# Kernel tuning notes

Hardware: AMD Instinct MI355X
Metric: run time of the kernel (lower is better)

The kernel has to match this reference:

```python
import math
import jax, jax.numpy as jnp
import numpy as np

B, S, E, H, DK, NW = 2048, 1, 1024, 128, 8, 8  # d_k == n_wires == 8, seq_len must be 1
DIM = 2 ** NW


def setup_inputs() -> dict:
    key = jax.random.key(0)
    ks = jax.random.split(key, 7)
    scale = 1.0 / math.sqrt(E)
    return {
        "x": jax.random.normal(ks[0], (B, S, E), jnp.float32),
        "wq": jax.random.normal(ks[1], (E, E), jnp.float32) * scale,
        "wk": jax.random.normal(ks[2], (E, E), jnp.float32) * scale,
        "wv": jax.random.normal(ks[3], (E, E), jnp.float32) * scale,
        "wc": jax.random.normal(ks[4], (E, E), jnp.float32) * scale,
        "bc": jax.random.normal(ks[5], (E,), jnp.float32) * 0.01,
        "rx_params": jax.random.normal(ks[6], (NW,), jnp.float32),  # trainable RX angles (shared q_layer)
    }


def _apply_rx(state, theta, wire):
    # state: (N, 2,...,2) [NW qubit axes]; theta: scalar or (N,)
    N = state.shape[0]
    theta = jnp.broadcast_to(theta, (N,))
    c = jnp.cos(theta * 0.5).astype(jnp.complex64)[:, None]
    s = (-1j * jnp.sin(theta * 0.5).astype(jnp.complex64))[:, None]
    st = jnp.moveaxis(state, wire + 1, 1).reshape(N, 2, -1)
    new = jnp.stack([c * st[:, 0] + s * st[:, 1],
                     s * st[:, 0] + c * st[:, 1]], axis=1)
    return jnp.moveaxis(new.reshape((N,) + (2,) * NW), 1, wire + 1)


def _apply_cnot(state, ctrl, tgt):
    st = jnp.moveaxis(state, (ctrl + 1, tgt + 1), (1, 2))
    st = jnp.stack([st[:, 0], jnp.flip(st[:, 1], axis=1)], axis=1)
    return jnp.moveaxis(st, (1, 2), (ctrl + 1, tgt + 1))


def _qlayer(angles, rx_params):
    # angles: (N, NW) per-sample RX encoder angles; rx_params: (NW,) shared trainable RX
    N = angles.shape[0]
    state = jnp.zeros((N,) + (2,) * NW, jnp.complex64)
    state = state.at[(slice(None),) + (0,) * NW].set(1.0 + 0j)  # |0...0>
    for w in range(NW):
        state = _apply_rx(state, angles[:, w], w)      # encoder RX(x_w)
    for w in range(NW):
        state = _apply_rx(state, rx_params[w], w)      # trainable RX
    for w in range(NW - 1):
        state = _apply_cnot(state, w, w + 1)           # CNOT chain
    state = _apply_cnot(state, NW - 1, 0)              # ring closure
    probs = jnp.abs(state.reshape(N, DIM)) ** 2
    bits = (jnp.arange(DIM)[:, None] >> jnp.arange(NW - 1, -1, -1)[None, :]) & 1  # wire 0 = MSB
    signs = (1.0 - 2.0 * bits).astype(jnp.float32)     # (DIM, NW)
    return probs @ signs                               # <Z_w> per wire, (N, NW)


def reference(x, wq, wk, wv, wc, bc, rx_params):
    q = jnp.einsum('bse,fe->bsf', x, wq).reshape(B, S, H, DK)
    k = jnp.einsum('bse,fe->bsf', x, wk).reshape(B, S, H, DK)
    v = jnp.einsum('bse,fe->bsf', x, wv).reshape(B, S, H, DK)
    scores = jnp.einsum('bqhd,bkhd->bhqk', q, k) / math.sqrt(DK)
    attn = jax.nn.softmax(scores, axis=-1)             # dropout is identity in eval
    out = jnp.einsum('bhqk,bkhd->bqhd', attn, v).reshape(B, S, E)
    # per-head quantum circuit (S==1, d_k==NW); batch all heads together
    angles = out.reshape(B * H, DK)
    qout = _qlayer(angles, rx_params).reshape(B, S, E)
    return jnp.einsum('bse,fe->bsf', qout, wc) + bc
```

## Files before the change

kernel.cpp:

```cpp
#include <hip/hip_runtime.h>
#include <hip/hip_bf16.h>
#include <math.h>


#define BB 2048
#define EN 1024

typedef short s16x8 __attribute__((ext_vector_type(8)));
typedef float f32x4 __attribute__((ext_vector_type(4)));

union Frag { s16x8 v; __hip_bfloat16 h[8]; };

__device__ inline s16x8 cvt_frag(f32x4 lo, f32x4 hi) {
    Frag u;
    #pragma unroll
    for (int j = 0; j < 4; ++j) {
        u.h[j]     = __float2bfloat16(lo[j]);
        u.h[4 + j] = __float2bfloat16(hi[j]);
    }
    return u.v;
}

__device__ inline void gll16(const __hip_bfloat16* g, __hip_bfloat16* l) {
    __builtin_amdgcn_global_load_lds(
        (const __attribute__((address_space(1))) void*)g,
        (__attribute__((address_space(3))) void*)l,
        16, 0, 0);
}

__global__ __launch_bounds__(256) void cvt3_kernel(
        const float* __restrict__ x, const float* __restrict__ wv,
        const float* __restrict__ wc,
        __hip_bfloat16* __restrict__ xb, __hip_bfloat16* __restrict__ wvb,
        __hip_bfloat16* __restrict__ wcb, int nx)
{
    const int g = blockIdx.x * 256 + threadIdx.x;
    const int NG = (EN * EN) / 8;
    const float* s; __hip_bfloat16* d; size_t off;
    if (g < nx)           { s = x;  d = xb;  off = (size_t)g * 8; }
    else if (g < nx + NG) { s = wv; d = wvb; off = (size_t)(g - nx) * 8; }
    else                  { s = wc; d = wcb; off = (size_t)(g - nx - NG) * 8; }
    f32x4 lo = *(const f32x4*)(s + off);
    f32x4 hi = *(const f32x4*)(s + off + 4);
    *(s16x8*)(d + off) = cvt_frag(lo, hi);
}

template <int EPI>
__global__ __launch_bounds__(256, 2) void gemm_kernel(
        const __hip_bfloat16* __restrict__ A,
        const __hip_bfloat16* __restrict__ W,
        const float* __restrict__ bias,
        void* __restrict__ Cv)
{
    __shared__ __hip_bfloat16 lds[16384];

    const int tid  = threadIdx.x;
    const int wave = tid >> 6, lane = tid & 63;
    const int l15 = lane & 15, lq = lane >> 4;
    const int m0 = blockIdx.x * 64, n0 = blockIdx.y * 64;
    const int wm = (wave & 1) * 32, wn = (wave >> 1) * 32;

    const __hip_bfloat16* gsrc[4];
    int ldst[4];
    #pragma unroll
    for (int i = 0; i < 4; ++i) {
        const int t  = wave * 4 + i;
        const int kt = t & 1;
        int row, lofs;
        const __hip_bfloat16* base;
        if (t < 8) { const int mt = t >> 1;       row = m0 + mt * 16 + l15; base = A; lofs = t * 512; }
        else       { const int nt = (t - 8) >> 1; row = n0 + nt * 16 + l15; base = W; lofs = 4096 + (t - 8) * 512; }
        gsrc[i] = base + (size_t)row * EN + kt * 32 + lq * 8;
        ldst[i] = lofs;
    }

    f32x4 acc[2][2] = {};

    #pragma unroll
    for (int i = 0; i < 4; ++i) gll16(gsrc[i], &lds[ldst[i]]);
    __syncthreads();

    int p = 0;
    for (int k0 = 64; k0 <= EN; k0 += 64) {
        if (k0 < EN) {
            const int q = p ^ 1;
            #pragma unroll
            for (int i = 0; i < 4; ++i) gll16(gsrc[i] + k0, &lds[q * 8192 + ldst[i]]);
        }
        const __hip_bfloat16* Ab = &lds[p * 8192];
        const __hip_bfloat16* Bb = Ab + 4096;
        #pragma unroll
        for (int kt = 0; kt < 2; ++kt) {
            s16x8 a[2], b[2];
            #pragma unroll
            for (int mi = 0; mi < 2; ++mi)
                a[mi] = *(const s16x8*)&Ab[((wm >> 4) + mi) * 1024 + kt * 512 + lane * 8];
            #pragma unroll
            for (int nj = 0; nj < 2; ++nj)
                b[nj] = *(const s16x8*)&Bb[((wn >> 4) + nj) * 1024 + kt * 512 + lane * 8];
            #pragma unroll
            for (int mi = 0; mi < 2; ++mi)
                #pragma unroll
                for (int nj = 0; nj < 2; ++nj)
                    acc[mi][nj] = __builtin_amdgcn_mfma_f32_16x16x32_bf16(
                                      a[mi], b[nj], acc[mi][nj], 0, 0, 0);
        }
        __syncthreads();
        p ^= 1;
    }

    if (EPI == 0) {
        __hip_bfloat16* C = (__hip_bfloat16*)Cv;
        #pragma unroll
        for (int mi = 0; mi < 2; ++mi)
            #pragma unroll
            for (int nj = 0; nj < 2; ++nj) {
                const int col = n0 + wn + nj * 16 + l15;
                #pragma unroll
                for (int r = 0; r < 4; ++r) {
                    const int row = m0 + wm + mi * 16 + lq * 4 + r;
                    C[(size_t)row * EN + col] = __float2bfloat16(acc[mi][nj][r]);
                }
            }
    } else {
        float* C = (float*)Cv;
        #pragma unroll
        for (int nj = 0; nj < 2; ++nj) {
            const int col = n0 + wn + nj * 16 + l15;
            const float bv = bias[col];
            #pragma unroll
            for (int mi = 0; mi < 2; ++mi)
                #pragma unroll
                for (int r = 0; r < 4; ++r) {
                    const int row = m0 + wm + mi * 16 + lq * 4 + r;
                    C[(size_t)row * EN + col] = acc[mi][nj][r] + bv;
                }
        }
    }
}

__global__ __launch_bounds__(256) void quantum_kernel(
        __hip_bfloat16* __restrict__ V, const float* __restrict__ rx)
{
    const int g = blockIdx.x * 256 + threadIdx.x;
    Frag in;
    in.v = *(const s16x8*)(V + (size_t)g * 8);
    float t[8];
    #pragma unroll
    for (int j = 0; j < 8; ++j)
        t[j] = cosf(__bfloat162float(in.h[j]) + rx[j]);

    Frag o;
    float suf = t[1];
    #pragma unroll
    for (int j = 2; j < 8; ++j) suf *= t[j];
    o.h[0] = __float2bfloat16(suf);
    float p = t[0];
    #pragma unroll
    for (int j = 1; j < 8; ++j) { p *= t[j]; o.h[j] = __float2bfloat16(p); }

    *(s16x8*)(V + (size_t)g * 8) = o.v;
}

extern "C" void kernel_launch(void* const* d_in, const int* in_sizes, int n_in,
                              void* d_out, int out_size, void* d_ws, size_t ws_size,
                              hipStream_t stream)
{
    const float* x  = (const float*)d_in[0];
    const float* wv = (const float*)d_in[3];
    const float* wc = (const float*)d_in[4];
    const float* bc = (const float*)d_in[5];
    const float* rx = (const float*)d_in[6];
    float* out = (float*)d_out;

    const size_t XE = (size_t)BB * EN;
    const size_t WE = (size_t)EN * EN;

    __hip_bfloat16* xb  = (__hip_bfloat16*)d_ws;
    __hip_bfloat16* wvb = xb + XE;
    __hip_bfloat16* wcb = wvb + WE;
    __hip_bfloat16* V   = wcb + WE;

    dim3 grid(BB / 64, EN / 64);
    cvt3_kernel<<<(int)((XE / 8 + 2 * (WE / 8)) / 256), 256, 0, stream>>>(
        x, wv, wc, xb, wvb, wcb, (int)(XE / 8));
    gemm_kernel<0><<<grid, 256, 0, stream>>>(xb, wvb, nullptr, V);
    quantum_kernel<<<(int)(XE / 8 / 256), 256, 0, stream>>>(V, rx);
    gemm_kernel<1><<<grid, 256, 0, stream>>>(V, wcb, bc, out);
}
```

Measured before the change: 116.2 us.

## Fuse convert, two GEMMs and quantum stage into one cooperative kernel

Replaces four separate kernel launches with a single cooperative kernel of 512 blocks that runs conversion, the first GEMM, the quantum cosine-product stage and the output GEMM, separated by grid-wide barriers. This targets launch overhead and inter-kernel gaps. It also swaps cosf for the faster, less accurate __cosf intrinsic. The cost is three grid.sync barriers, and the grid must be fully co-resident (512 blocks at 2 per CU), which limits flexibility.

```diff
diff --git a/kernel.cpp b/kernel.cpp
--- a/kernel.cpp
+++ b/kernel.cpp
@@ -1,10 +1,13 @@
 #include <hip/hip_runtime.h>
+#include <hip/hip_cooperative_groups.h>
 #include <hip/hip_bf16.h>
 #include <math.h>
 
 
 #define BB 2048
 #define EN 1024
+
+namespace cg = cooperative_groups;
 
 typedef short s16x8 __attribute__((ext_vector_type(8)));
 typedef float f32x4 __attribute__((ext_vector_type(4)));
@@ -28,36 +31,16 @@
         16, 0, 0);
 }
 
-__global__ __launch_bounds__(256) void cvt3_kernel(
-        const float* __restrict__ x, const float* __restrict__ wv,
-        const float* __restrict__ wc,
-        __hip_bfloat16* __restrict__ xb, __hip_bfloat16* __restrict__ wvb,
-        __hip_bfloat16* __restrict__ wcb, int nx)
+template <int EPI>
+__device__ void gemm_tile(const __hip_bfloat16* __restrict__ A,
+                          const __hip_bfloat16* __restrict__ W,
+                          const float* __restrict__ bias,
+                          void* __restrict__ Cv,
+                          int m0, int n0, int tid,
+                          __hip_bfloat16* lds)
 {
-    const int g = blockIdx.x * 256 + threadIdx.x;
-    const int NG = (EN * EN) / 8;
-    const float* s; __hip_bfloat16* d; size_t off;
-    if (g < nx)           { s = x;  d = xb;  off = (size_t)g * 8; }
-    else if (g < nx + NG) { s = wv; d = wvb; off = (size_t)(g - nx) * 8; }
-    else                  { s = wc; d = wcb; off = (size_t)(g - nx - NG) * 8; }
-    f32x4 lo = *(const f32x4*)(s + off);
-    f32x4 hi = *(const f32x4*)(s + off + 4);
-    *(s16x8*)(d + off) = cvt_frag(lo, hi);
-}
-
-template <int EPI>
-__global__ __launch_bounds__(256, 2) void gemm_kernel(
-        const __hip_bfloat16* __restrict__ A,
-        const __hip_bfloat16* __restrict__ W,
-        const float* __restrict__ bias,
-        void* __restrict__ Cv)
-{
-    __shared__ __hip_bfloat16 lds[16384];
-
-    const int tid  = threadIdx.x;
     const int wave = tid >> 6, lane = tid & 63;
     const int l15 = lane & 15, lq = lane >> 4;
-    const int m0 = blockIdx.x * 64, n0 = blockIdx.y * 64;
     const int wm = (wave & 1) * 32, wn = (wave >> 1) * 32;
 
     const __hip_bfloat16* gsrc[4];
@@ -139,27 +122,65 @@
     }
 }
 
-__global__ __launch_bounds__(256) void quantum_kernel(
-        __hip_bfloat16* __restrict__ V, const float* __restrict__ rx)
+__global__ __launch_bounds__(256, 2) void fused_kernel(
+        const float* __restrict__ x,  const float* __restrict__ wv,
+        const float* __restrict__ wc, const float* __restrict__ bc,
+        const float* __restrict__ rx, float* __restrict__ out,
+        __hip_bfloat16* __restrict__ xb, __hip_bfloat16* __restrict__ wvb,
+        __hip_bfloat16* __restrict__ wcb, __hip_bfloat16* __restrict__ V)
 {
-    const int g = blockIdx.x * 256 + threadIdx.x;
-    Frag in;
-    in.v = *(const s16x8*)(V + (size_t)g * 8);
-    float t[8];
-    #pragma unroll
-    for (int j = 0; j < 8; ++j)
-        t[j] = cosf(__bfloat162float(in.h[j]) + rx[j]);
-
-    Frag o;
-    float suf = t[1];
-    #pragma unroll
-    for (int j = 2; j < 8; ++j) suf *= t[j];
-    o.h[0] = __float2bfloat16(suf);
-    float p = t[0];
-    #pragma unroll
-    for (int j = 1; j < 8; ++j) { p *= t[j]; o.h[j] = __float2bfloat16(p); }
-
-    *(s16x8*)(V + (size_t)g * 8) = o.v;
+    cg::grid_group grid = cg::this_grid();
+    __shared__ __hip_bfloat16 lds[16384];
+
+    const int tid = threadIdx.x;
+    const int bid = blockIdx.x;
+    const int tg  = bid * 256 + tid;
+
+    {
+        #pragma unroll
+        for (int r = 0; r < 4; ++r) {
+            const float* s = (r < 2) ? x : (r == 2 ? wv : wc);
+            __hip_bfloat16* d = (r < 2) ? xb : (r == 2 ? wvb : wcb);
+            const size_t off = ((size_t)tg + (r == 1 ? 131072u : 0u)) * 8;
+            f32x4 lo = *(const f32x4*)(s + off);
+            f32x4 hi = *(const f32x4*)(s + off + 4);
+            *(s16x8*)(d + off) = cvt_frag(lo, hi);
+        }
+    }
+    grid.sync();
+
+    const int m0 = (bid >> 4) * 64;
+    const int n0 = (bid & 15) * 64;
+    gemm_tile<0>(xb, wvb, nullptr, V, m0, n0, tid, lds);
+    grid.sync();
+
+    {
+        float rxl[8];
+        #pragma unroll
+        for (int j = 0; j < 8; ++j) rxl[j] = rx[j];
+        #pragma unroll
+        for (int r = 0; r < 2; ++r) {
+            const size_t g = (size_t)tg + (size_t)r * 131072u;
+            Frag in;
+            in.v = *(const s16x8*)(V + g * 8);
+            float t[8];
+            #pragma unroll
+            for (int j = 0; j < 8; ++j)
+                t[j] = __cosf(__bfloat162float(in.h[j]) + rxl[j]);
+            Frag o;
+            float suf = t[1];
+            #pragma unroll
+            for (int j = 2; j < 8; ++j) suf *= t[j];
+            o.h[0] = __float2bfloat16(suf);
+            float p = t[0];
+            #pragma unroll
+            for (int j = 1; j < 8; ++j) { p *= t[j]; o.h[j] = __float2bfloat16(p); }
+            *(s16x8*)(V + g * 8) = o.v;
+        }
+    }
+    grid.sync();
+
+    gemm_tile<1>(V, wcb, bc, out, m0, n0, tid, lds);
 }
 
 extern "C" void kernel_launch(void* const* d_in, const int* in_sizes, int n_in,
@@ -181,10 +202,8 @@
     __hip_bfloat16* wcb = wvb + WE;
     __hip_bfloat16* V   = wcb + WE;
 
-    dim3 grid(BB / 64, EN / 64);
-    cvt3_kernel<<<(int)((XE / 8 + 2 * (WE / 8)) / 256), 256, 0, stream>>>(
-        x, wv, wc, xb, wvb, wcb, (int)(XE / 8));
-    gemm_kernel<0><<<grid, 256, 0, stream>>>(xb, wvb, nullptr, V);
-    quantum_kernel<<<(int)(XE / 8 / 256), 256, 0, stream>>>(V, rx);
-    gemm_kernel<1><<<grid, 256, 0, stream>>>(V, wcb, bc, out);
-}
+    void* args[] = { (void*)&x, (void*)&wv, (void*)&wc, (void*)&bc, (void*)&rx,
+                     (void*)&out, (void*)&xb, (void*)&wvb, (void*)&wcb, (void*)&V };
+    hipLaunchCooperativeKernel((const void*)fused_kernel,
+                               dim3(512), dim3(256), args, 0, stream);
+}
```

Result: slower. 319.5 us (+174.9%).

## Fuse V-projection, quantum layer and output GEMM into one row-block kernel

Applied to the files above, without the earlier changes.

Replaces the separate x conversion, first GEMM, quantum elementwise kernel and second GEMM with one kernel per 16-row block. Each block converts its x rows to bf16 in LDS, computes all 1024 V columns, applies the closed-form quantum cosine-product in LDS, then runs the output GEMM and adds the bias. This removes the global round trips for xb and V and three kernel launches. In exchange only 128 blocks run, each streaming the full weight matrices from global or L2 without LDS tiling, which risks low occupancy and weight-bandwidth limits. It also switches cosf to the faster, less accurate __cosf.

```diff
diff --git a/kernel.cpp b/kernel.cpp
--- a/kernel.cpp
+++ b/kernel.cpp
@@ -3,8 +3,8 @@
 #include <math.h>
 
 
-#define BB 2048
 #define EN 1024
+#define ROWS 16
 
 typedef short s16x8 __attribute__((ext_vector_type(8)));
 typedef float f32x4 __attribute__((ext_vector_type(4)));
@@ -21,145 +21,118 @@
     return u.v;
 }
 
-__device__ inline void gll16(const __hip_bfloat16* g, __hip_bfloat16* l) {
-    __builtin_amdgcn_global_load_lds(
-        (const __attribute__((address_space(1))) void*)g,
-        (__attribute__((address_space(3))) void*)l,
-        16, 0, 0);
-}
-
-__global__ __launch_bounds__(256) void cvt3_kernel(
-        const float* __restrict__ x, const float* __restrict__ wv,
-        const float* __restrict__ wc,
-        __hip_bfloat16* __restrict__ xb, __hip_bfloat16* __restrict__ wvb,
-        __hip_bfloat16* __restrict__ wcb, int nx)
+__global__ __launch_bounds__(256) void cvtw_kernel(
+        const float* __restrict__ wv, const float* __restrict__ wc,
+        __hip_bfloat16* __restrict__ wvb, __hip_bfloat16* __restrict__ wcb)
 {
     const int g = blockIdx.x * 256 + threadIdx.x;
     const int NG = (EN * EN) / 8;
-    const float* s; __hip_bfloat16* d; size_t off;
-    if (g < nx)           { s = x;  d = xb;  off = (size_t)g * 8; }
-    else if (g < nx + NG) { s = wv; d = wvb; off = (size_t)(g - nx) * 8; }
-    else                  { s = wc; d = wcb; off = (size_t)(g - nx - NG) * 8; }
+    const float* s = (g < NG) ? wv : wc;
+    __hip_bfloat16* d = (g < NG) ? wvb : wcb;
+    const size_t off = (size_t)((g < NG) ? g : g - NG) * 8;
     f32x4 lo = *(const f32x4*)(s + off);
     f32x4 hi = *(const f32x4*)(s + off + 4);
     *(s16x8*)(d + off) = cvt_frag(lo, hi);
 }
 
-template <int EPI>
-__global__ __launch_bounds__(256, 2) void gemm_kernel(
-        const __hip_bfloat16* __restrict__ A,
-        const __hip_bfloat16* __restrict__ W,
-        const float* __restrict__ bias,
-        void* __restrict__ Cv)
+__global__ __launch_bounds__(512, 2) void fused_kernel(
+        const float* __restrict__ x,
+        const __hip_bfloat16* __restrict__ wvb,
+        const __hip_bfloat16* __restrict__ wcb,
+        const float* __restrict__ bc, const float* __restrict__ rx,
+        float* __restrict__ out)
 {
-    __shared__ __hip_bfloat16 lds[16384];
+    __shared__ __hip_bfloat16 xs[32 * 64 * 8];
+    __shared__ __hip_bfloat16 vs[ROWS * 1032];
 
     const int tid  = threadIdx.x;
     const int wave = tid >> 6, lane = tid & 63;
     const int l15 = lane & 15, lq = lane >> 4;
-    const int m0 = blockIdx.x * 64, n0 = blockIdx.y * 64;
-    const int wm = (wave & 1) * 32, wn = (wave >> 1) * 32;
+    const int m0 = blockIdx.x * ROWS;
 
-    const __hip_bfloat16* gsrc[4];
-    int ldst[4];
-    #pragma unroll
-    for (int i = 0; i < 4; ++i) {
-        const int t  = wave * 4 + i;
-        const int kt = t & 1;
-        int row, lofs;
-        const __hip_bfloat16* base;
-        if (t < 8) { const int mt = t >> 1;       row = m0 + mt * 16 + l15; base = A; lofs = t * 512; }
-        else       { const int nt = (t - 8) >> 1; row = n0 + nt * 16 + l15; base = W; lofs = 4096 + (t - 8) * 512; }
-        gsrc[i] = base + (size_t)row * EN + kt * 32 + lq * 8;
-        ldst[i] = lofs;
+    {
+        const int r = tid & 15, lq2 = (tid >> 4) & 3, kc0 = tid >> 6;
+        #pragma unroll
+        for (int p = 0; p < 4; ++p) {
+            const int kc = kc0 + 8 * p;
+            const int k  = kc * 32 + lq2 * 8;
+            const float* px = x + (size_t)(m0 + r) * EN + k;
+            f32x4 lo = *(const f32x4*)px;
+            f32x4 hi = *(const f32x4*)(px + 4);
+            *(s16x8*)&xs[(size_t)(kc * 64 + lq2 * 16 + r) * 8] = cvt_frag(lo, hi);
+        }
     }
-
-    f32x4 acc[2][2] = {};
-
-    #pragma unroll
-    for (int i = 0; i < 4; ++i) gll16(gsrc[i], &lds[ldst[i]]);
     __syncthreads();
 
-    int p = 0;
-    for (int k0 = 64; k0 <= EN; k0 += 64) {
-        if (k0 < EN) {
-            const int q = p ^ 1;
+    {
+        f32x4 acc[8] = {};
+        const __hip_bfloat16* wb = wvb + (size_t)(wave * 128 + l15) * EN + lq * 8;
+        for (int kc = 0; kc < 32; ++kc) {
+            s16x8 a = *(const s16x8*)&xs[(size_t)(kc * 64 + lane) * 8];
             #pragma unroll
-            for (int i = 0; i < 4; ++i) gll16(gsrc[i] + k0, &lds[q * 8192 + ldst[i]]);
+            for (int nf = 0; nf < 8; ++nf) {
+                s16x8 b = *(const s16x8*)(wb + (size_t)nf * 16 * EN + kc * 32);
+                acc[nf] = __builtin_amdgcn_mfma_f32_16x16x32_bf16(a, b, acc[nf], 0, 0, 0);
+            }
         }
-        const __hip_bfloat16* Ab = &lds[p * 8192];
-        const __hip_bfloat16* Bb = Ab + 4096;
         #pragma unroll
-        for (int kt = 0; kt < 2; ++kt) {
-            s16x8 a[2], b[2];
+        for (int nf = 0; nf < 8; ++nf) {
+            const int col = wave * 128 + nf * 16 + l15;
             #pragma unroll
-            for (int mi = 0; mi < 2; ++mi)
-                a[mi] = *(const s16x8*)&Ab[((wm >> 4) + mi) * 1024 + kt * 512 + lane * 8];
-            #pragma unroll
-            for (int nj = 0; nj < 2; ++nj)
-                b[nj] = *(const s16x8*)&Bb[((wn >> 4) + nj) * 1024 + kt * 512 + lane * 8];
-            #pragma unroll
-            for (int mi = 0; mi < 2; ++mi)
-                #pragma unroll
-                for (int nj = 0; nj < 2; ++nj)
-                    acc[mi][nj] = __builtin_amdgcn_mfma_f32_16x16x32_bf16(
-                                      a[mi], b[nj], acc[mi][nj], 0, 0, 0);
-        }
-        __syncthreads();
-        p ^= 1;
-    }
-
-    if (EPI == 0) {
-        __hip_bfloat16* C = (__hip_bfloat16*)Cv;
-        #pragma unroll
-        for (int mi = 0; mi < 2; ++mi)
-            #pragma unroll
-            for (int nj = 0; nj < 2; ++nj) {
-                const int col = n0 + wn + nj * 16 + l15;
-                #pragma unroll
-                for (int r = 0; r < 4; ++r) {
-                    const int row = m0 + wm + mi * 16 + lq * 4 + r;
-                    C[(size_t)row * EN + col] = __float2bfloat16(acc[mi][nj][r]);
-                }
-            }
-    } else {
-        float* C = (float*)Cv;
-        #pragma unroll
-        for (int nj = 0; nj < 2; ++nj) {
-            const int col = n0 + wn + nj * 16 + l15;
-            const float bv = bias[col];
-            #pragma unroll
-            for (int mi = 0; mi < 2; ++mi)
-                #pragma unroll
-                for (int r = 0; r < 4; ++r) {
-                    const int row = m0 + wm + mi * 16 + lq * 4 + r;
-                    C[(size_t)row * EN + col] = acc[mi][nj][r] + bv;
-                }
+            for (int r = 0; r < 4; ++r)
+                vs[(lq * 4 + r) * 1032 + col] = __float2bfloat16(acc[nf][r]);
         }
     }
-}
+    __syncthreads();
 
-__global__ __launch_bounds__(256) void quantum_kernel(
-        __hip_bfloat16* __restrict__ V, const float* __restrict__ rx)
-{
-    const int g = blockIdx.x * 256 + threadIdx.x;
-    Frag in;
-    in.v = *(const s16x8*)(V + (size_t)g * 8);
-    float t[8];
-    #pragma unroll
-    for (int j = 0; j < 8; ++j)
-        t[j] = cosf(__bfloat162float(in.h[j]) + rx[j]);
+    {
+        float rxl[8];
+        #pragma unroll
+        for (int j = 0; j < 8; ++j) rxl[j] = rx[j];
+        #pragma unroll
+        for (int p = 0; p < 4; ++p) {
+            const int idx = p * 512 + tid;
+            const int g = idx >> 4, r = idx & 15;
+            Frag in;
+            in.v = *(const s16x8*)&vs[r * 1032 + g * 8];
+            float t[8];
+            #pragma unroll
+            for (int j = 0; j < 8; ++j)
+                t[j] = __cosf(__bfloat162float(in.h[j]) + rxl[j]);
+            Frag o;
+            float suf = t[1];
+            #pragma unroll
+            for (int j = 2; j < 8; ++j) suf *= t[j];
+            o.h[0] = __float2bfloat16(suf);
+            float pr = t[0];
+            #pragma unroll
+            for (int j = 1; j < 8; ++j) { pr *= t[j]; o.h[j] = __float2bfloat16(pr); }
+            const int kc = g >> 2, lq2 = g & 3;
+            *(s16x8*)&xs[(size_t)(kc * 64 + lq2 * 16 + r) * 8] = o.v;
+        }
+    }
+    __syncthreads();
 
-    Frag o;
-    float suf = t[1];
-    #pragma unroll
-    for (int j = 2; j < 8; ++j) suf *= t[j];
-    o.h[0] = __float2bfloat16(suf);
-    float p = t[0];
-    #pragma unroll
-    for (int j = 1; j < 8; ++j) { p *= t[j]; o.h[j] = __float2bfloat16(p); }
-
-    *(s16x8*)(V + (size_t)g * 8) = o.v;
+    {
+        f32x4 acc[8] = {};
+        const __hip_bfloat16* wb = wcb + (size_t)(wave * 128 + l15) * EN + lq * 8;
+        for (int kc = 0; kc < 32; ++kc) {
+            s16x8 a = *(const s16x8*)&xs[(size_t)(kc * 64 + lane) * 8];
+            #pragma unroll
+            for (int nf = 0; nf < 8; ++nf) {
+                s16x8 b = *(const s16x8*)(wb + (size_t)nf * 16 * EN + kc * 32);
+                acc[nf] = __builtin_amdgcn_mfma_f32_16x16x32_bf16(a, b, acc[nf], 0, 0, 0);
+            }
+        }
+        #pragma unroll
+        for (int nf = 0; nf < 8; ++nf) {
+            const int col = wave * 128 + nf * 16 + l15;
+            const float bv = bc[col];
+            #pragma unroll
+            for (int r = 0; r < 4; ++r)
+                out[(size_t)(m0 + lq * 4 + r) * EN + col] = acc[nf][r] + bv;
+        }
+    }
 }
 
 extern "C" void kernel_launch(void* const* d_in, const int* in_sizes, int n_in,
@@ -173,18 +146,10 @@
     const float* rx = (const float*)d_in[6];
     float* out = (float*)d_out;
 
-    const size_t XE = (size_t)BB * EN;
     const size_t WE = (size_t)EN * EN;
+    __hip_bfloat16* wvb = (__hip_bfloat16*)d_ws;
+    __hip_bfloat16* wcb = wvb + WE;
 
-    __hip_bfloat16* xb  = (__hip_bfloat16*)d_ws;
-    __hip_bfloat16* wvb = xb + XE;
-    __hip_bfloat16* wcb = wvb + WE;
-    __hip_bfloat16* V   = wcb + WE;
-
-    dim3 grid(BB / 64, EN / 64);
-    cvt3_kernel<<<(int)((XE / 8 + 2 * (WE / 8)) / 256), 256, 0, stream>>>(
-        x, wv, wc, xb, wvb, wcb, (int)(XE / 8));
-    gemm_kernel<0><<<grid, 256, 0, stream>>>(xb, wvb, nullptr, V);
-    quantum_kernel<<<(int)(XE / 8 / 256), 256, 0, stream>>>(V, rx);
-    gemm_kernel<1><<<grid, 256, 0, stream>>>(V, wcb, bc, out);
+    cvtw_kernel<<<(int)(2 * (WE / 8) / 256), 256, 0, stream>>>(wv, wc, wvb, wcb);
+    fused_kernel<<<2048 / ROWS, 512, 0, stream>>>(x, wvb, wcb, bc, rx, out);
 }
```

Result: slower. 194.2 us (+67.1%).

## Fuse quantum cosine-product into first GEMM epilogue and use 8-wave blocks

Applied to the files above, without the earlier changes.

Removes the standalone quantum kernel by staging the first GEMM's fp32 tile in shared memory and applying the cos/prefix-product circuit in the epilogue, writing bf16 results once. The GEMM blocks grow from 4 to 8 waves, each wave computing a 16x32 sub-tile, with per-wave loads halved. This avoids one launch and a full read/write round trip of the intermediate, and skips the bf16 rounding before the cosine. It also switches to the fast __cosf intrinsic, which costs some accuracy, and the smaller per-wave tiles lower MFMA work per LDS read.

```diff
diff --git a/kernel.cpp b/kernel.cpp
--- a/kernel.cpp
+++ b/kernel.cpp
@@ -32,52 +32,54 @@
         const float* __restrict__ x, const float* __restrict__ wv,
         const float* __restrict__ wc,
         __hip_bfloat16* __restrict__ xb, __hip_bfloat16* __restrict__ wvb,
-        __hip_bfloat16* __restrict__ wcb, int nx)
+        __hip_bfloat16* __restrict__ wcb)
 {
     const int g = blockIdx.x * 256 + threadIdx.x;
+    const int NX = (BB * EN) / 8;
     const int NG = (EN * EN) / 8;
     const float* s; __hip_bfloat16* d; size_t off;
-    if (g < nx)           { s = x;  d = xb;  off = (size_t)g * 8; }
-    else if (g < nx + NG) { s = wv; d = wvb; off = (size_t)(g - nx) * 8; }
-    else                  { s = wc; d = wcb; off = (size_t)(g - nx - NG) * 8; }
+    if (g < NX)           { s = x;  d = xb;  off = (size_t)g * 8; }
+    else if (g < NX + NG) { s = wv; d = wvb; off = (size_t)(g - NX) * 8; }
+    else                  { s = wc; d = wcb; off = (size_t)(g - NX - NG) * 8; }
     f32x4 lo = *(const f32x4*)(s + off);
     f32x4 hi = *(const f32x4*)(s + off + 4);
     *(s16x8*)(d + off) = cvt_frag(lo, hi);
 }
 
 template <int EPI>
-__global__ __launch_bounds__(256, 2) void gemm_kernel(
+__global__ __launch_bounds__(512, 4) void gemm_kernel(
         const __hip_bfloat16* __restrict__ A,
         const __hip_bfloat16* __restrict__ W,
-        const float* __restrict__ bias,
+        const float* __restrict__ bias, const float* __restrict__ rx,
         void* __restrict__ Cv)
 {
-    __shared__ __hip_bfloat16 lds[16384];
+    __shared__ __align__(16) unsigned char smem[32768];
+    __hip_bfloat16* lds = (__hip_bfloat16*)smem;
 
     const int tid  = threadIdx.x;
     const int wave = tid >> 6, lane = tid & 63;
     const int l15 = lane & 15, lq = lane >> 4;
     const int m0 = blockIdx.x * 64, n0 = blockIdx.y * 64;
-    const int wm = (wave & 1) * 32, wn = (wave >> 1) * 32;
+    const int wmt = wave >> 1;
+    const int wnt = wave & 1;
 
-    const __hip_bfloat16* gsrc[4];
-    int ldst[4];
+    const __hip_bfloat16* gsrc[2];
+    int ldst[2];
     #pragma unroll
-    for (int i = 0; i < 4; ++i) {
-        const int t  = wave * 4 + i;
-        const int kt = t & 1;
+    for (int i = 0; i < 2; ++i) {
+        const int t = wave * 2 + i;
         int row, lofs;
         const __hip_bfloat16* base;
-        if (t < 8) { const int mt = t >> 1;       row = m0 + mt * 16 + l15; base = A; lofs = t * 512; }
-        else       { const int nt = (t - 8) >> 1; row = n0 + nt * 16 + l15; base = W; lofs = 4096 + (t - 8) * 512; }
-        gsrc[i] = base + (size_t)row * EN + kt * 32 + lq * 8;
+        if (t < 8) { const int mt = t >> 1; row = m0 + mt * 16 + l15; base = A; lofs = t * 512; }
+        else       { const int u = t - 8;   row = n0 + (u >> 1) * 16 + l15; base = W; lofs = 4096 + u * 512; }
+        gsrc[i] = base + (size_t)row * EN + (t & 1) * 32 + lq * 8;
         ldst[i] = lofs;
     }
 
-    f32x4 acc[2][2] = {};
+    f32x4 acc[2] = {};
 
     #pragma unroll
-    for (int i = 0; i < 4; ++i) gll16(gsrc[i], &lds[ldst[i]]);
+    for (int i = 0; i < 2; ++i) gll16(gsrc[i], &lds[ldst[i]]);
     __syncthreads();
 
     int p = 0;
@@ -85,81 +87,61 @@
         if (k0 < EN) {
             const int q = p ^ 1;
             #pragma unroll
-            for (int i = 0; i < 4; ++i) gll16(gsrc[i] + k0, &lds[q * 8192 + ldst[i]]);
+            for (int i = 0; i < 2; ++i) gll16(gsrc[i] + k0, &lds[q * 8192 + ldst[i]]);
         }
         const __hip_bfloat16* Ab = &lds[p * 8192];
         const __hip_bfloat16* Bb = Ab + 4096;
         #pragma unroll
         for (int kt = 0; kt < 2; ++kt) {
-            s16x8 a[2], b[2];
+            s16x8 a = *(const s16x8*)&Ab[(wmt * 2 + kt) * 512 + lane * 8];
             #pragma unroll
-            for (int mi = 0; mi < 2; ++mi)
-                a[mi] = *(const s16x8*)&Ab[((wm >> 4) + mi) * 1024 + kt * 512 + lane * 8];
-            #pragma unroll
-            for (int nj = 0; nj < 2; ++nj)
-                b[nj] = *(const s16x8*)&Bb[((wn >> 4) + nj) * 1024 + kt * 512 + lane * 8];
-            #pragma unroll
-            for (int mi = 0; mi < 2; ++mi)
-                #pragma unroll
-                for (int nj = 0; nj < 2; ++nj)
-                    acc[mi][nj] = __builtin_amdgcn_mfma_f32_16x16x32_bf16(
-                                      a[mi], b[nj], acc[mi][nj], 0, 0, 0);
+            for (int j = 0; j < 2; ++j) {
+                s16x8 b = *(const s16x8*)&Bb[((wnt * 2 + j) * 2 + kt) * 512 + lane * 8];
+                acc[j] = __builtin_amdgcn_mfma_f32_16x16x32_bf16(a, b, acc[j], 0, 0, 0);
+            }
         }
         __syncthreads();
         p ^= 1;
     }
 
     if (EPI == 0) {
-        __hip_bfloat16* C = (__hip_bfloat16*)Cv;
+        float* sb = (float*)smem;
         #pragma unroll
-        for (int mi = 0; mi < 2; ++mi)
+        for (int j = 0; j < 2; ++j) {
+            const int col = wnt * 32 + j * 16 + l15;
             #pragma unroll
-            for (int nj = 0; nj < 2; ++nj) {
-                const int col = n0 + wn + nj * 16 + l15;
-                #pragma unroll
-                for (int r = 0; r < 4; ++r) {
-                    const int row = m0 + wm + mi * 16 + lq * 4 + r;
-                    C[(size_t)row * EN + col] = __float2bfloat16(acc[mi][nj][r]);
-                }
-            }
+            for (int r = 0; r < 4; ++r)
+                sb[(wmt * 16 + lq * 4 + r) * 68 + col] = acc[j][r];
+        }
+        __syncthreads();
+        const int row = tid >> 3, g = tid & 7;
+        const float* pv = &sb[row * 68 + g * 8];
+        float t[8];
+        #pragma unroll
+        for (int j = 0; j < 8; ++j) t[j] = __cosf(pv[j] + rx[j]);
+        Frag o;
+        float suf = t[1];
+        #pragma unroll
+        for (int j = 2; j < 8; ++j) suf *= t[j];
+        o.h[0] = __float2bfloat16(suf);
+        float pr = t[0];
+        #pragma unroll
+        for (int j = 1; j < 8; ++j) { pr *= t[j]; o.h[j] = __float2bfloat16(pr); }
+        __hip_bfloat16* V = (__hip_bfloat16*)Cv;
+        *(s16x8*)(V + (size_t)(m0 + row) * EN + n0 + g * 8) = o.v;
     } else {
         float* C = (float*)Cv;
         #pragma unroll
-        for (int nj = 0; nj < 2; ++nj) {
-            const int col = n0 + wn + nj * 16 + l15;
+        for (int j = 0; j < 2; ++j) {
+            const int col = n0 + wnt * 32 + j * 16 + l15;
             const float bv = bias[col];
             #pragma unroll
-            for (int mi = 0; mi < 2; ++mi)
-                #pragma unroll
-                for (int r = 0; r < 4; ++r) {
-                    const int row = m0 + wm + mi * 16 + lq * 4 + r;
-                    C[(size_t)row * EN + col] = acc[mi][nj][r] + bv;
-                }
+            for (int r = 0; r < 4; ++r) {
+                const int row = m0 + wmt * 16 + lq * 4 + r;
+                C[(size_t)row * EN + col] = acc[j][r] + bv;
+            }
         }
     }
-}
-
-__global__ __launch_bounds__(256) void quantum_kernel(
-        __hip_bfloat16* __restrict__ V, const float* __restrict__ rx)
-{
-    const int g = blockIdx.x * 256 + threadIdx.x;
-    Frag in;
-    in.v = *(const s16x8*)(V + (size_t)g * 8);
-    float t[8];
-    #pragma unroll
-    for (int j = 0; j < 8; ++j)
-        t[j] = cosf(__bfloat162float(in.h[j]) + rx[j]);
-
-    Frag o;
-    float suf = t[1];
-    #pragma unroll
-    for (int j = 2; j < 8; ++j) suf *= t[j];
-    o.h[0] = __float2bfloat16(suf);
-    float p = t[0];
-    #pragma unroll
-    for (int j = 1; j < 8; ++j) { p *= t[j]; o.h[j] = __float2bfloat16(p); }
-
-    *(s16x8*)(V + (size_t)g * 8) = o.v;
 }
 
 extern "C" void kernel_launch(void* const* d_in, const int* in_sizes, int n_in,
@@ -183,8 +165,7 @@
 
     dim3 grid(BB / 64, EN / 64);
     cvt3_kernel<<<(int)((XE / 8 + 2 * (WE / 8)) / 256), 256, 0, stream>>>(
-        x, wv, wc, xb, wvb, wcb, (int)(XE / 8));
-    gemm_kernel<0><<<grid, 256, 0, stream>>>(xb, wvb, nullptr, V);
-    quantum_kernel<<<(int)(XE / 8 / 256), 256, 0, stream>>>(V, rx);
-    gemm_kernel<1><<<grid, 256, 0, stream>>>(V, wcb, bc, out);
+        x, wv, wc, xb, wvb, wcb);
+    gemm_kernel<0><<<grid, 512, 0, stream>>>(xb, wvb, nullptr, rx, V);
+    gemm_kernel<1><<<grid, 512, 0, stream>>>(V, wcb, bc, nullptr, out);
 }
```

After: 112.3 us. 3.4% less time.
